# Kernel tuning notes

Measured on AMD Instinct MI355X. Metric: run time of the kernel, lower is better.

Reference implementation:

```python
import jax, jax.numpy as jnp
import numpy as np

B, S, HID = 2, 2048, 1024
NH, DK, DV = 4, 256, 256   # head_k_dim = head_v_dim = 1024 / 4
KSZ = 4                    # conv_size
EPS = 1e-5


def causal_conv1d(x, w):
    # x: [B, S, C] channels-last, w: [C, K] depthwise kernel (torch [C,1,K] squeezed)
    K = w.shape[1]
    Sn = x.shape[1]
    xp = jnp.pad(x, ((0, 0), (K - 1, 0), (0, 0)))
    # cross-correlation with left padding K-1 -> causal: out[t] = sum_j w[:,j] * x[t-(K-1)+j]
    out = xp[:, 0:Sn, :] * w[:, 0]
    for j in range(1, K):
        out = out + xp[:, j:j + Sn, :] * w[:, j]
    return out


def l2norm(x, eps=1e-6):
    return x * jax.lax.rsqrt(jnp.sum(x * x, axis=-1, keepdims=True) + eps)


def rms_norm(x, w, eps=EPS):
    return x * jax.lax.rsqrt(jnp.mean(x * x, axis=-1, keepdims=True) + eps) * w


def delta_rule(q, k, v, beta):
    # q,k: [B,S,H,dk]; v: [B,S,H,dv]; beta: [B,S,H]
    Bn, Sn, Hn, dk = q.shape
    dv = v.shape[-1]
    N = Bn * Hn
    qs = jnp.moveaxis(q, 1, 0).reshape(Sn, N, dk)
    ks = jnp.moveaxis(k, 1, 0).reshape(Sn, N, dk)
    vs = jnp.moveaxis(v, 1, 0).reshape(Sn, N, dv)
    bs = jnp.moveaxis(beta, 1, 0).reshape(Sn, N)

    S0 = jnp.zeros((N, dk, dv), q.dtype)

    def step(St, inp):
        qt, kt, vt, bt = inp
        kS = jnp.einsum('nk,nkv->nv', kt, St)              # k^T S
        St = St + jnp.einsum('nk,nv->nkv', kt, bt[:, None] * (vt - kS))
        ot = jnp.einsum('nk,nkv->nv', qt, St)
        return St, ot

    _, o = jax.lax.scan(step, S0, (qs, ks, vs, bs))        # o: [S, N, dv]
    o = o.reshape(Sn, Bn, Hn, dv)
    return jnp.moveaxis(o, 0, 1)                            # [B,S,H,dv]


def setup_inputs() -> dict:
    key = jax.random.key(0)
    ks = jax.random.split(key, 10)
    w_scale = 2.0 ** (-2.5) * np.sqrt(6.0 / (HID + HID))   # xavier_uniform with gain 2^-2.5
    u = lambda k, shp, s: jax.random.uniform(k, shp, jnp.float32, -s, s)
    return {
        'hidden_states': jax.random.normal(ks[0], (B, S, HID), jnp.float32),
        'Wq': u(ks[1], (HID, NH * DK), w_scale),
        'Wk': u(ks[2], (HID, NH * DK), w_scale),
        'Wv': u(ks[3], (HID, NH * DV), w_scale),
        'Wb': u(ks[4], (HID, NH), w_scale),
        'conv_q': jax.random.normal(ks[5], (NH * DK, KSZ), jnp.float32) * 0.2,
        'conv_k': jax.random.normal(ks[6], (NH * DK, KSZ), jnp.float32) * 0.2,
        'conv_v': jax.random.normal(ks[7], (NH * DV, KSZ), jnp.float32) * 0.2,
        'norm_w': jnp.ones((DV,), jnp.float32),
        'Wo': u(ks[8], (NH * DV, HID), w_scale),
    }


def reference(hidden_states, Wq, Wk, Wv, Wb, conv_q, conv_k, conv_v, norm_w, Wo):
    q = hidden_states @ Wq                                  # [B,S,key_dim]
    k = hidden_states @ Wk
    v = hidden_states @ Wv
    q = causal_conv1d(q, conv_q)
    k = causal_conv1d(k, conv_k)
    v = causal_conv1d(v, conv_v)
    q = jax.nn.silu(q).reshape(B, S, NH, DK)
    k = jax.nn.silu(k).reshape(B, S, NH, DK)
    v = jax.nn.silu(v).reshape(B, S, NH, DV)
    beta = jax.nn.sigmoid(hidden_states @ Wb)               # [B,S,H]
    q = l2norm(q)
    k = l2norm(k)
    o = delta_rule(q, k, v, beta)                           # [B,S,H,dv]
    o = rms_norm(o, norm_w)
    o = o.reshape(B, S, NH * DV) @ Wo                       # [B,S,HID]
    return o
```

## Files before the change

kernel.cpp:

```cpp
#include <hip/hip_runtime.h>
#include <math.h>

#define BB   2
#define SS   2048
#define HIDD 1024
#define ROWS 4096
#define NCH  32
#define CH   64

typedef unsigned short u16t;
typedef unsigned int   u32t;

typedef __attribute__((ext_vector_type(8))) short bf16x8;
typedef __attribute__((ext_vector_type(4))) float f32x4;

__device__ __forceinline__ float bf2f(u16t u) { return __uint_as_float(((u32t)u) << 16); }
__device__ __forceinline__ u16t f2bf(float f) {
    u32t b = __float_as_uint(f);
    return (u16t)((b + 0x7FFFu + ((b >> 16) & 1u)) >> 16);
}
__device__ __forceinline__ float lo_bf(u32t u) { return __uint_as_float(u << 16); }
__device__ __forceinline__ float hi_bf(u32t u) { return __uint_as_float(u & 0xFFFF0000u); }

__device__ __forceinline__ float waveReduceSum(float v) {
#pragma unroll
    for (int m = 1; m < 64; m <<= 1) v += __shfl_xor(v, m, 64);
    return v;
}

__device__ __forceinline__ void gload16(const void* g, void* l) {
    __builtin_amdgcn_global_load_lds(
        (const __attribute__((address_space(1))) unsigned int*)g,
        (__attribute__((address_space(3))) unsigned int*)l, 16, 0, 0);
}

#define MFMA(a, b, c) __builtin_amdgcn_mfma_f32_16x16x32_bf16(a, b, c, 0, 0, 0)

__global__ __launch_bounds__(256) void f2bf_kernel(const float* __restrict__ in,
                                                   u16t* __restrict__ out) {
    const size_t idx = ((size_t)blockIdx.x * 256 + threadIdx.x) * 8;
    float4 a = *(const float4*)&in[idx];
    float4 b = *(const float4*)&in[idx + 4];
    ushort4 o1, o2;
    o1.x = f2bf(a.x); o1.y = f2bf(a.y); o1.z = f2bf(a.z); o1.w = f2bf(a.w);
    o2.x = f2bf(b.x); o2.y = f2bf(b.y); o2.z = f2bf(b.z); o2.w = f2bf(b.w);
    *(ushort4*)&out[idx] = o1;
    *(ushort4*)&out[idx + 4] = o2;
}

__global__ __launch_bounds__(256) void transpose_w4(const float* __restrict__ W0,
                                                    const float* __restrict__ W1,
                                                    const float* __restrict__ W2,
                                                    const float* __restrict__ W3,
                                                    u16t* __restrict__ T0,
                                                    u16t* __restrict__ T1,
                                                    u16t* __restrict__ T2,
                                                    u16t* __restrict__ T3) {
    __shared__ u16t tile[64][65];
    const int z = blockIdx.z;
    const float* W = (z == 0) ? W0 : (z == 1) ? W1 : (z == 2) ? W2 : W3;
    u16t* WT = (z == 0) ? T0 : (z == 1) ? T1 : (z == 2) ? T2 : T3;
    const int t = threadIdx.x;
    const int r0 = blockIdx.y * 64, c0 = blockIdx.x * 64;
    const int lr = t >> 2, lc4 = (t & 3) * 16;
#pragma unroll
    for (int m = 0; m < 4; ++m) {
        float4 v = *(const float4*)&W[(size_t)(r0 + lr) * 1024 + c0 + lc4 + m * 4];
        tile[lr][lc4 + m * 4 + 0] = f2bf(v.x);
        tile[lr][lc4 + m * 4 + 1] = f2bf(v.y);
        tile[lr][lc4 + m * 4 + 2] = f2bf(v.z);
        tile[lr][lc4 + m * 4 + 3] = f2bf(v.w);
    }
    __syncthreads();
#pragma unroll
    for (int m = 0; m < 16; ++m)
        WT[(size_t)(c0 + lr) * 1024 + r0 + lc4 + m] = tile[lc4 + m][lr];
}

__global__ __launch_bounds__(256) void gemm_mfma(const u16t* __restrict__ A,
                                                 const u16t* __restrict__ BT,
                                                 float* __restrict__ Cf,
                                                 u16t* __restrict__ Cb, int obf,
                                                 int M, int N, int K,
                                                 size_t bStrideP, size_t cStrideP) {
    __shared__ u16t As[128 * 64];
    __shared__ u16t Bs[128 * 64];
    const int t = threadIdx.x, l = t & 63, w = t >> 6;
    const int wr = w >> 1, wc = w & 1;
    const int rowBase = blockIdx.y * 128, colBase = blockIdx.x * 128;
    const int l15 = l & 15, g4 = l >> 4;

    const int bplane = colBase >> 10;
    const int bcol = colBase & 1023;

    const int srow = l >> 3;
    const int sj = (l & 7) ^ srow;
    const u16t* aSrc = A + (size_t)(rowBase + srow) * K + sj * 8;
    const u16t* bSrc = BT + (size_t)bplane * bStrideP + (size_t)(bcol + srow) * K + sj * 8;

    f32x4 acc[4][4];
#pragma unroll
    for (int i = 0; i < 4; ++i)
#pragma unroll
        for (int j = 0; j < 4; ++j) acc[i][j] = (f32x4){0.f, 0.f, 0.f, 0.f};

    for (int k0 = 0; k0 < K; k0 += 64) {
#pragma unroll
        for (int i = 0; i < 4; ++i) {
            const int rb = (i * 4 + w) * 8;
            gload16(aSrc + (size_t)rb * K + k0, &As[rb * 64]);
            gload16(bSrc + (size_t)rb * K + k0, &Bs[rb * 64]);
        }
        __syncthreads();
#pragma unroll
        for (int kh = 0; kh < 2; ++kh) {
            bf16x8 aF[4], bF[4];
#pragma unroll
            for (int mi = 0; mi < 4; ++mi) {
                const int row = wr * 64 + mi * 16 + l15;
                const int phys = (kh * 4 + g4) ^ (row & 7);
                aF[mi] = *(const bf16x8*)&As[row * 64 + phys * 8];
            }
#pragma unroll
            for (int ni = 0; ni < 4; ++ni) {
                const int row = wc * 64 + ni * 16 + l15;
                const int phys = (kh * 4 + g4) ^ (row & 7);
                bF[ni] = *(const bf16x8*)&Bs[row * 64 + phys * 8];
            }
#pragma unroll
            for (int mi = 0; mi < 4; ++mi)
#pragma unroll
                for (int ni = 0; ni < 4; ++ni)
                    acc[mi][ni] = MFMA(aF[mi], bF[ni], acc[mi][ni]);
        }
        __syncthreads();
    }
#pragma unroll
    for (int mi = 0; mi < 4; ++mi)
#pragma unroll
        for (int ni = 0; ni < 4; ++ni)
#pragma unroll
            for (int rg = 0; rg < 4; ++rg) {
                const int row = rowBase + wr * 64 + mi * 16 + g4 * 4 + rg;
                const int col = colBase + wc * 64 + ni * 16 + l15;
                const int plane = col >> 10, cc = col & 1023;
                const float v = acc[mi][ni][rg];
                if (obf) Cb[(size_t)plane * cStrideP + (size_t)row * 1024 + cc] = f2bf(v);
                else     Cf[(size_t)plane * cStrideP + (size_t)row * 1024 + cc] = v;
            }
}

__global__ __launch_bounds__(256) void beta_kernel(const float* __restrict__ X,
                                                   const float* __restrict__ Wb,
                                                   float* __restrict__ beta) {
    const int gw   = (blockIdx.x * blockDim.x + threadIdx.x) >> 6;
    const int lane = threadIdx.x & 63;
    if (gw >= ROWS) return;
    const float* x = X + (size_t)gw * HIDD;
    float a0 = 0.f, a1 = 0.f, a2 = 0.f, a3 = 0.f;
#pragma unroll
    for (int i = 0; i < 4; ++i) {
        const int k = lane * 16 + i * 4;
        float4 xv = *(const float4*)&x[k];
        float4 w0 = *(const float4*)&Wb[(size_t)(k + 0) * 4];
        float4 w1 = *(const float4*)&Wb[(size_t)(k + 1) * 4];
        float4 w2 = *(const float4*)&Wb[(size_t)(k + 2) * 4];
        float4 w3 = *(const float4*)&Wb[(size_t)(k + 3) * 4];
        a0 += xv.x * w0.x + xv.y * w1.x + xv.z * w2.x + xv.w * w3.x;
        a1 += xv.x * w0.y + xv.y * w1.y + xv.z * w2.y + xv.w * w3.y;
        a2 += xv.x * w0.z + xv.y * w1.z + xv.z * w2.z + xv.w * w3.z;
        a3 += xv.x * w0.w + xv.y * w1.w + xv.z * w2.w + xv.w * w3.w;
    }
    a0 = waveReduceSum(a0); a1 = waveReduceSum(a1);
    a2 = waveReduceSum(a2); a3 = waveReduceSum(a3);
    if (lane == 0) {
        float4 o = make_float4(1.f / (1.f + expf(-a0)), 1.f / (1.f + expf(-a1)),
                               1.f / (1.f + expf(-a2)), 1.f / (1.f + expf(-a3)));
        *(float4*)&beta[(size_t)gw * 4] = o;
    }
}

__global__ __launch_bounds__(256) void conv_qv(const u16t* __restrict__ inQ,
                                               const float* __restrict__ wQ,
                                               u16t* __restrict__ outQ,
                                               const u16t* __restrict__ inV,
                                               const float* __restrict__ wV,
                                               u16t* __restrict__ outV) {
    const int isQ = (blockIdx.y == 0);
    const u16t* in = isQ ? inQ : inV;
    const float* w = isQ ? wQ : wV;
    u16t* out      = isQ ? outQ : outV;
    const int doL2 = isQ;

    const int gw   = (blockIdx.x * blockDim.x + threadIdx.x) >> 6;
    const int lane = threadIdx.x & 63;
    const int r = gw >> 2;
    const int h = gw & 3;
    const int b = r >> 11;
    const int s = r & 2047;
    const int c4 = h * 256 + lane * 4;

    const float4 wr0 = *(const float4*)&w[(size_t)(c4 + 0) * 4];
    const float4 wr1 = *(const float4*)&w[(size_t)(c4 + 1) * 4];
    const float4 wr2 = *(const float4*)&w[(size_t)(c4 + 2) * 4];
    const float4 wr3 = *(const float4*)&w[(size_t)(c4 + 3) * 4];

    const size_t rowB = (size_t)(b << 11);
    float x0[4] = {0, 0, 0, 0}, x1[4] = {0, 0, 0, 0}, x2[4] = {0, 0, 0, 0}, x3[4];
    ushort4 u;
    if (s >= 3) { u = *(const ushort4*)&in[(rowB + s - 3) * HIDD + c4];
        x0[0] = bf2f(u.x); x0[1] = bf2f(u.y); x0[2] = bf2f(u.z); x0[3] = bf2f(u.w); }
    if (s >= 2) { u = *(const ushort4*)&in[(rowB + s - 2) * HIDD + c4];
        x1[0] = bf2f(u.x); x1[1] = bf2f(u.y); x1[2] = bf2f(u.z); x1[3] = bf2f(u.w); }
    if (s >= 1) { u = *(const ushort4*)&in[(rowB + s - 1) * HIDD + c4];
        x2[0] = bf2f(u.x); x2[1] = bf2f(u.y); x2[2] = bf2f(u.z); x2[3] = bf2f(u.w); }
    u = *(const ushort4*)&in[(rowB + s) * HIDD + c4];
    x3[0] = bf2f(u.x); x3[1] = bf2f(u.y); x3[2] = bf2f(u.z); x3[3] = bf2f(u.w);

    float y0 = wr0.x * x0[0] + wr0.y * x1[0] + wr0.z * x2[0] + wr0.w * x3[0];
    float y1 = wr1.x * x0[1] + wr1.y * x1[1] + wr1.z * x2[1] + wr1.w * x3[1];
    float y2 = wr2.x * x0[2] + wr2.y * x1[2] + wr2.z * x2[2] + wr2.w * x3[2];
    float y3 = wr3.x * x0[3] + wr3.y * x1[3] + wr3.z * x2[3] + wr3.w * x3[3];

    y0 = y0 / (1.f + expf(-y0)); y1 = y1 / (1.f + expf(-y1));
    y2 = y2 / (1.f + expf(-y2)); y3 = y3 / (1.f + expf(-y3));

    if (doL2) {
        float ss = y0 * y0 + y1 * y1 + y2 * y2 + y3 * y3;
        ss = waveReduceSum(ss);
        float sc = rsqrtf(ss + 1e-6f);
        y0 *= sc; y1 *= sc; y2 *= sc; y3 *= sc;
    }
    ushort4 o;
    o.x = f2bf(y0); o.y = f2bf(y1); o.z = f2bf(y2); o.w = f2bf(y3);
    *(ushort4*)&out[(size_t)r * HIDD + c4] = o;
}

__global__ __launch_bounds__(256) void conv_k_chunk(const u16t* __restrict__ pre,
                                                    const float* __restrict__ w,
                                                    u16t* __restrict__ rowout,
                                                    u16t* __restrict__ trout) {
    const int t = threadIdx.x;
    const int bh = blockIdx.x >> 5, c = blockIdx.x & 31;
    const int b = bh >> 2, h = bh & 3;
    const int i = t >> 2, g = t & 3;
    const int s = c * 64 + i;
    const size_t row = (size_t)b * 2048 + s;
    const int ch0 = h * 256 + g * 64;
    const int cloc = g * 64;
    float y[64];
#pragma unroll
    for (int m = 0; m < 8; ++m) {
        const int cm = ch0 + m * 8;
        uint4 x3 = *(const uint4*)&pre[row * 1024 + cm];
        uint4 x2 = (s >= 1) ? *(const uint4*)&pre[(row - 1) * 1024 + cm] : make_uint4(0, 0, 0, 0);
        uint4 x1 = (s >= 2) ? *(const uint4*)&pre[(row - 2) * 1024 + cm] : make_uint4(0, 0, 0, 0);
        uint4 x0 = (s >= 3) ? *(const uint4*)&pre[(row - 3) * 1024 + cm] : make_uint4(0, 0, 0, 0);
        u32t c0[4] = {x0.x, x0.y, x0.z, x0.w};
        u32t c1[4] = {x1.x, x1.y, x1.z, x1.w};
        u32t c2[4] = {x2.x, x2.y, x2.z, x2.w};
        u32t c3[4] = {x3.x, x3.y, x3.z, x3.w};
#pragma unroll
        for (int p = 0; p < 4; ++p) {
            const int ch = m * 8 + p * 2;
            float4 wA = *(const float4*)&w[(size_t)(ch0 + ch) * 4];
            float4 wB = *(const float4*)&w[(size_t)(ch0 + ch + 1) * 4];
            float ya = wA.x * lo_bf(c0[p]) + wA.y * lo_bf(c1[p]) + wA.z * lo_bf(c2[p]) + wA.w * lo_bf(c3[p]);
            float yb = wB.x * hi_bf(c0[p]) + wB.y * hi_bf(c1[p]) + wB.z * hi_bf(c2[p]) + wB.w * hi_bf(c3[p]);
            ya = ya / (1.f + expf(-ya));
            yb = yb / (1.f + expf(-yb));
            y[ch] = ya; y[ch + 1] = yb;
        }
    }
    float ss = 0.f;
#pragma unroll
    for (int e = 0; e < 64; ++e) ss += y[e] * y[e];
    ss += __shfl_xor(ss, 1);
    ss += __shfl_xor(ss, 2);
    const float sc = rsqrtf(ss + 1e-6f);
#pragma unroll
    for (int m = 0; m < 8; ++m) {
        uint4 o;
        u32t* op = (u32t*)&o;
#pragma unroll
        for (int p = 0; p < 4; ++p) {
            u16t a = f2bf(y[m * 8 + p * 2] * sc);
            u16t bb2 = f2bf(y[m * 8 + p * 2 + 1] * sc);
            op[p] = (u32t)a | ((u32t)bb2 << 16);
        }
        *(uint4*)&rowout[row * 1024 + ch0 + m * 8] = o;
    }
#pragma unroll
    for (int e = 0; e < 64; ++e)
        trout[((size_t)bh * 256 + cloc + e) * 2048 + s] = f2bf(y[e] * sc);
}

__global__ __launch_bounds__(256) void prep_kernel(const u16t* __restrict__ qcb,
                                                   const u16t* __restrict__ kcb,
                                                   const float* __restrict__ beta,
                                                   u16t* __restrict__ Tghi,
                                                   u16t* __restrict__ Tglo,
                                                   u16t* __restrict__ Agb) {
    __shared__ float KT[256][68];
    __shared__ float QT[256][68];
    __shared__ float Af[64][68];
    const int t = threadIdx.x;
    const int bhc = blockIdx.x;
    const int bh = bhc >> 5, c = bhc & 31;
    const int b = bh >> 2, h = bh & 3;
    const int tb = b * SS + c * CH;

    {
        const int i = t & 63, rb = t >> 6;
        const u16t* kg = kcb + (size_t)(tb + i) * HIDD + h * 256 + rb * 64;
        const u16t* qg = qcb + (size_t)(tb + i) * HIDD + h * 256 + rb * 64;
#pragma unroll
        for (int m = 0; m < 8; ++m) {
            uint4 kv = ((const uint4*)kg)[m];
            uint4 qv = ((const uint4*)qg)[m];
            u32t kw[4] = {kv.x, kv.y, kv.z, kv.w};
            u32t qw[4] = {qv.x, qv.y, qv.z, qv.w};
#pragma unroll
            for (int n = 0; n < 4; ++n) {
                int rr = rb * 64 + m * 8 + n * 2;
                KT[rr][i]     = lo_bf(kw[n]);
                KT[rr + 1][i] = hi_bf(kw[n]);
                QT[rr][i]     = lo_bf(qw[n]);
                QT[rr + 1][i] = hi_bf(qw[n]);
            }
        }
    }
    __syncthreads();

    const int it = t & 63, jb = t >> 6;
    float kk[16], qk[16];
#pragma unroll
    for (int m = 0; m < 16; ++m) { kk[m] = 0.f; qk[m] = 0.f; }
#pragma unroll 2
    for (int r = 0; r < 256; ++r) {
        float ki = KT[r][it];
        float qi = QT[r][it];
        float4 ka = *(const float4*)&KT[r][jb * 16 + 0];
        float4 kb = *(const float4*)&KT[r][jb * 16 + 4];
        float4 kc = *(const float4*)&KT[r][jb * 16 + 8];
        float4 kd = *(const float4*)&KT[r][jb * 16 + 12];
        float kj[16] = {ka.x, ka.y, ka.z, ka.w, kb.x, kb.y, kb.z, kb.w,
                        kc.x, kc.y, kc.z, kc.w, kd.x, kd.y, kd.z, kd.w};
#pragma unroll
        for (int m = 0; m < 16; ++m) { kk[m] += ki * kj[m]; qk[m] += qi * kj[m]; }
    }

    const float bta = beta[(size_t)(tb + it) * 4 + h];
    u16t* ag = Agb + (size_t)bhc * 4096 + (size_t)it * 64 + jb * 16;
#pragma unroll
    for (int m = 0; m < 16; ++m) {
        int j = jb * 16 + m;
        Af[it][j] = (j < it) ? bta * kk[m] : 0.f;
    }
#pragma unroll
    for (int m4 = 0; m4 < 4; ++m4) {
        ushort4 o;
        o.x = f2bf((jb * 16 + m4 * 4 + 0 <= it) ? qk[m4 * 4 + 0] : 0.f);
        o.y = f2bf((jb * 16 + m4 * 4 + 1 <= it) ? qk[m4 * 4 + 1] : 0.f);
        o.z = f2bf((jb * 16 + m4 * 4 + 2 <= it) ? qk[m4 * 4 + 2] : 0.f);
        o.w = f2bf((jb * 16 + m4 * 4 + 3 <= it) ? qk[m4 * 4 + 3] : 0.f);
        *(ushort4*)&ag[m4 * 4] = o;
    }
    __syncthreads();

    if (t < 64) {
        const int ccol = t;
        float tc[64];
#pragma unroll
        for (int j = 0; j < 64; ++j) tc[j] = (j == ccol) ? 1.f : 0.f;
#pragma unroll
        for (int i = 1; i < 64; ++i) {
            float a = 0.f;
#pragma unroll
            for (int j = 0; j < i; ++j) a += Af[i][j] * tc[j];
            tc[i] -= a;
        }
        u16t* th = Tghi + (size_t)bhc * 4096;
        u16t* tl = Tglo + (size_t)bhc * 4096;
#pragma unroll
        for (int i = 0; i < 64; ++i) {
            u16t hi = f2bf(tc[i]);
            th[i * 64 + ccol] = hi;
            tl[i * 64 + ccol] = f2bf(tc[i] - bf2f(hi));
        }
    }
}

__global__ __launch_bounds__(256, 1) void scan_mfma(const u16t* __restrict__ qcb,
                                                    const u16t* __restrict__ kcb,
                                                    const u16t* __restrict__ ktr,
                                                    const u16t* __restrict__ vcb,
                                                    const float* __restrict__ beta,
                                                    const u16t* __restrict__ TghiG,
                                                    const u16t* __restrict__ TgloG,
                                                    const u16t* __restrict__ AgbG,
                                                    u16t* __restrict__ o_raw) {
    __shared__ u16t Shi[16 * 256];
    __shared__ u16t Slo[16 * 256];
    __shared__ u16t Rhi[16 * 64];
    __shared__ u16t Rlo[16 * 64];
    __shared__ u16t Uhi[16 * 64];
    __shared__ u16t Ulo[16 * 64];

    const int t = threadIdx.x, l = t & 63, w = t >> 6;
    const int bh = blockIdx.x & 7, vt = blockIdx.x >> 3;
    const int b = bh >> 2, h = bh & 3;
    const int vcol0 = vt * 16;
    const int vlow = l & 15, g4 = l >> 4;

    for (int i = t; i < 16 * 256; i += 256) { Shi[i] = 0; Slo[i] = 0; }
    f32x4 sf[4];
#pragma unroll
    for (int q = 0; q < 4; ++q) sf[q] = (f32x4){0.f, 0.f, 0.f, 0.f};

    bf16x8 kf[8], qf[8], tfh[2], tfl[2], af[2], kcf[8];
    u16t vfb[4];
    float bta[4];

    auto loadKQ = [&](int c) {
        const size_t rb = (size_t)(b * 2048 + c * 64 + 16 * w + vlow) * 1024 + h * 256 + g4 * 8;
#pragma unroll
        for (int ks = 0; ks < 8; ++ks) {
            kf[ks] = *(const bf16x8*)(kcb + rb + ks * 32);
            qf[ks] = *(const bf16x8*)(qcb + rb + ks * 32);
        }
    };
    auto loadVB = [&](int c) {
        const int r0 = b * 2048 + c * 64 + 16 * w + 4 * g4;
#pragma unroll
        for (int rg = 0; rg < 4; ++rg) {
            vfb[rg] = vcb[(size_t)(r0 + rg) * 1024 + h * 256 + vcol0 + vlow];
            bta[rg] = beta[(size_t)(r0 + rg) * 4 + h];
        }
    };
    auto loadT = [&](int c) {
        const size_t tb2 = (size_t)(bh * 32 + c) * 4096 + (size_t)(16 * w + vlow) * 64 + g4 * 8;
        tfh[0] = *(const bf16x8*)(TghiG + tb2);
        tfh[1] = *(const bf16x8*)(TghiG + tb2 + 32);
        tfl[0] = *(const bf16x8*)(TgloG + tb2);
        tfl[1] = *(const bf16x8*)(TgloG + tb2 + 32);
    };
    auto loadA = [&](int c) {
        const size_t tb2 = (size_t)(bh * 32 + c) * 4096 + (size_t)(16 * w + vlow) * 64 + g4 * 8;
        af[0] = *(const bf16x8*)(AgbG + tb2);
        af[1] = *(const bf16x8*)(AgbG + tb2 + 32);
    };
    auto loadKC = [&](int c) {
        const size_t cb2 = ((size_t)bh * 256 + 64 * w + vlow) * 2048 + c * 64 + g4 * 8;
#pragma unroll
        for (int q2 = 0; q2 < 4; ++q2) {
            kcf[q2 * 2 + 0] = *(const bf16x8*)(ktr + cb2 + (size_t)(16 * q2) * 2048);
            kcf[q2 * 2 + 1] = *(const bf16x8*)(ktr + cb2 + (size_t)(16 * q2) * 2048 + 32);
        }
    };

    loadKQ(0); loadVB(0); loadT(0); loadA(0); loadKC(0);
    __syncthreads();

    for (int c = 0; c < NCH; ++c) {
        const int cn = (c + 1 < NCH) ? c + 1 : c;
        const int trow0 = b * 2048 + c * 64;

        f32x4 Wacc = (f32x4){0.f, 0.f, 0.f, 0.f};
        f32x4 O1   = (f32x4){0.f, 0.f, 0.f, 0.f};
#pragma unroll
        for (int ks = 0; ks < 8; ++ks) {
            const int pb = (((ks * 4 + g4) ^ (vlow & 7)) << 3);
            bf16x8 bH = *(const bf16x8*)&Shi[vlow * 256 + pb];
            bf16x8 bL = *(const bf16x8*)&Slo[vlow * 256 + pb];
            Wacc = MFMA(kf[ks], bH, Wacc); Wacc = MFMA(kf[ks], bL, Wacc);
            O1   = MFMA(qf[ks], bH, O1);   O1   = MFMA(qf[ks], bL, O1);
        }
        {
            const int tslot = 2 * w + (g4 >> 1);
            const int base = vlow * 64 + ((tslot ^ (vlow & 7)) << 3) + ((g4 & 1) << 2);
            u16t rh[4], rl[4];
#pragma unroll
            for (int rg = 0; rg < 4; ++rg) {
                float rv = bta[rg] * (bf2f(vfb[rg]) - Wacc[rg]);
                rh[rg] = f2bf(rv);
                rl[rg] = f2bf(rv - bf2f(rh[rg]));
            }
            uint2 ph, pl;
            ph.x = (u32t)rh[0] | ((u32t)rh[1] << 16); ph.y = (u32t)rh[2] | ((u32t)rh[3] << 16);
            pl.x = (u32t)rl[0] | ((u32t)rl[1] << 16); pl.y = (u32t)rl[2] | ((u32t)rl[3] << 16);
            *(uint2*)&Rhi[base] = ph;
            *(uint2*)&Rlo[base] = pl;
        }
        loadKQ(cn);
        loadVB(cn);
        __syncthreads();

        f32x4 Uacc = (f32x4){0.f, 0.f, 0.f, 0.f};
#pragma unroll
        for (int ks = 0; ks < 2; ++ks) {
            const int pb = (((ks * 4 + g4) ^ (vlow & 7)) << 3);
            bf16x8 bH = *(const bf16x8*)&Rhi[vlow * 64 + pb];
            bf16x8 bL = *(const bf16x8*)&Rlo[vlow * 64 + pb];
            Uacc = MFMA(tfh[ks], bH, Uacc);
            Uacc = MFMA(tfh[ks], bL, Uacc);
            Uacc = MFMA(tfl[ks], bH, Uacc);
        }
        {
            const int tslot = 2 * w + (g4 >> 1);
            const int base = vlow * 64 + ((tslot ^ (vlow & 7)) << 3) + ((g4 & 1) << 2);
            u16t uh[4], ul[4];
#pragma unroll
            for (int rg = 0; rg < 4; ++rg) {
                uh[rg] = f2bf(Uacc[rg]);
                ul[rg] = f2bf(Uacc[rg] - bf2f(uh[rg]));
            }
            uint2 ph, pl;
            ph.x = (u32t)uh[0] | ((u32t)uh[1] << 16); ph.y = (u32t)uh[2] | ((u32t)uh[3] << 16);
            pl.x = (u32t)ul[0] | ((u32t)ul[1] << 16); pl.y = (u32t)ul[2] | ((u32t)ul[3] << 16);
            *(uint2*)&Uhi[base] = ph;
            *(uint2*)&Ulo[base] = pl;
        }
        loadT(cn);
        __syncthreads();

        bf16x8 uhf[2], ulf[2];
#pragma unroll
        for (int ks = 0; ks < 2; ++ks) {
            const int pb = (((ks * 4 + g4) ^ (vlow & 7)) << 3);
            uhf[ks] = *(const bf16x8*)&Uhi[vlow * 64 + pb];
            ulf[ks] = *(const bf16x8*)&Ulo[vlow * 64 + pb];
        }
        f32x4 Oacc = O1;
#pragma unroll
        for (int ks = 0; ks < 2; ++ks) {
            Oacc = MFMA(af[ks], uhf[ks], Oacc);
            Oacc = MFMA(af[ks], ulf[ks], Oacc);
        }
#pragma unroll
        for (int rg = 0; rg < 4; ++rg)
            o_raw[(size_t)(trow0 + 16 * w + 4 * g4 + rg) * 1024 + h * 256 + vcol0 + vlow] = f2bf(Oacc[rg]);
        loadA(cn);

#pragma unroll
        for (int q = 0; q < 4; ++q) {
#pragma unroll
            for (int ks = 0; ks < 2; ++ks) {
                sf[q] = MFMA(kcf[q * 2 + ks], uhf[ks], sf[q]);
                sf[q] = MFMA(kcf[q * 2 + ks], ulf[ks], sf[q]);
            }
        }
        loadKC(cn);

#pragma unroll
        for (int q = 0; q < 4; ++q) {
            u16t sh[4], sl[4];
#pragma unroll
            for (int rg = 0; rg < 4; ++rg) {
                u16t hi = f2bf(sf[q][rg]);
                sh[rg] = hi;
                sl[rg] = f2bf(sf[q][rg] - bf2f(hi));
            }
            const int rslot = 8 * w + 2 * q + (g4 >> 1);
            const int base = vlow * 256 + ((rslot ^ (vlow & 7)) << 3) + ((g4 & 1) << 2);
            uint2 ph, pl;
            ph.x = (u32t)sh[0] | ((u32t)sh[1] << 16); ph.y = (u32t)sh[2] | ((u32t)sh[3] << 16);
            pl.x = (u32t)sl[0] | ((u32t)sl[1] << 16); pl.y = (u32t)sl[2] | ((u32t)sl[3] << 16);
            *(uint2*)&Shi[base] = ph;
            *(uint2*)&Slo[base] = pl;
        }
        __syncthreads();
    }
}

__global__ __launch_bounds__(256) void rms_kernel(const u16t* __restrict__ in,
                                                  const float* __restrict__ w,
                                                  u16t* __restrict__ out) {
    const int gw   = (blockIdx.x * blockDim.x + threadIdx.x) >> 6;
    const int lane = threadIdx.x & 63;
    const int r = gw >> 2;
    const int h = gw & 3;
    const size_t base = (size_t)r * HIDD + h * 256 + lane * 4;
    ushort4 xv = *(const ushort4*)&in[base];
    float x0 = bf2f(xv.x), x1 = bf2f(xv.y), x2 = bf2f(xv.z), x3 = bf2f(xv.w);
    float ss = x0 * x0 + x1 * x1 + x2 * x2 + x3 * x3;
    ss = waveReduceSum(ss);
    const float sc = rsqrtf(ss * (1.0f / 256.0f) + 1e-5f);
    float4 wv = *(const float4*)&w[lane * 4];
    ushort4 o;
    o.x = f2bf(x0 * sc * wv.x); o.y = f2bf(x1 * sc * wv.y);
    o.z = f2bf(x2 * sc * wv.z); o.w = f2bf(x3 * sc * wv.w);
    *(ushort4*)&out[base] = o;
}

extern "C" void kernel_launch(void* const* d_in, const int* in_sizes, int n_in,
                              void* d_out, int out_size, void* d_ws, size_t ws_size,
                              hipStream_t stream) {
    const float* X      = (const float*)d_in[0];
    const float* Wq     = (const float*)d_in[1];
    const float* Wk     = (const float*)d_in[2];
    const float* Wv     = (const float*)d_in[3];
    const float* Wb     = (const float*)d_in[4];
    const float* conv_q = (const float*)d_in[5];
    const float* conv_k = (const float*)d_in[6];
    const float* conv_v = (const float*)d_in[7];
    const float* norm_w = (const float*)d_in[8];
    const float* Wo     = (const float*)d_in[9];
    float* out = (float*)d_out;

    char* W8 = (char*)d_ws;
    const size_t MB = 1u << 20;
    u16t* Xbf   = (u16t*)(W8 + 0 * MB);
    u16t* o_raw = Xbf;
    u16t* qpre  = (u16t*)(W8 + 8 * MB);
    u16t* o_nrm = qpre;
    u16t* kpre  = (u16t*)(W8 + 16 * MB);
    u16t* Tghi  = (u16t*)(W8 + 16 * MB);
    u16t* Tglo  = (u16t*)(W8 + 18 * MB);
    u16t* Agb   = (u16t*)(W8 + 20 * MB);
    u16t* vpre  = (u16t*)(W8 + 24 * MB);
    u16t* ktr   = (u16t*)(W8 + 24 * MB);
    u16t* WqT   = (u16t*)(W8 + 32 * MB);
    u16t* qcb   = (u16t*)(W8 + 32 * MB);
    u16t* WkT   = (u16t*)(W8 + 40 * MB);
    u16t* kcb   = (u16t*)(W8 + 40 * MB);
    u16t* WvT   = (u16t*)(W8 + 48 * MB);
    u16t* vcb   = (u16t*)(W8 + 48 * MB);
    u16t* WoT   = (u16t*)(W8 + 56 * MB);
    float* betab = (float*)(W8 + 58 * MB);

    const size_t PL = 4194304;

    f2bf_kernel<<<2048, 256, 0, stream>>>(X, Xbf);
    transpose_w4<<<dim3(16, 16, 4), 256, 0, stream>>>(Wq, Wk, Wv, Wo, WqT, WkT, WvT, WoT);

    gemm_mfma<<<dim3(24, 32), 256, 0, stream>>>(Xbf, WqT, nullptr, qpre, 1,
                                                ROWS, 3072, HIDD, PL, PL);
    beta_kernel<<<ROWS / 4, 256, 0, stream>>>(X, Wb, betab);

    conv_qv<<<dim3(ROWS, 2), 256, 0, stream>>>(qpre, conv_q, qcb, vpre, conv_v, vcb);
    conv_k_chunk<<<256, 256, 0, stream>>>(kpre, conv_k, kcb, ktr);

    prep_kernel<<<256, 256, 0, stream>>>(qcb, kcb, betab, Tghi, Tglo, Agb);
    scan_mfma<<<128, 256, 0, stream>>>(qcb, kcb, ktr, vcb, betab, Tghi, Tglo, Agb, o_raw);

    rms_kernel<<<ROWS, 256, 0, stream>>>(o_raw, norm_w, o_nrm);
    gemm_mfma<<<dim3(8, 32), 256, 0, stream>>>(o_nrm, WoT, out, nullptr, 0,
                                               ROWS, HIDD, HIDD, 0, 0);
}
```

Measured before the change: 286.7 us.

## Pack four value-tile groups into one 1024-thread scan block

The chunked delta-rule scan now launches 32 blocks of 1024 threads instead of 128 blocks of 256. Each block holds four independent 4-wave groups, one per 16-column value tile, each with its own slice of shared state. Groups with the same (b,h) share the same K/Q/T/A chunk data, so cache reuse may improve. The cost is that __syncthreads now makes all 16 waves wait on each other even though the groups are independent, and only 32 CUs are occupied.

```diff
diff --git a/kernel.cpp b/kernel.cpp
--- a/kernel.cpp
+++ b/kernel.cpp
@@ -391,29 +391,38 @@
     }
 }
 
-__global__ __launch_bounds__(256, 1) void scan_mfma(const u16t* __restrict__ qcb,
-                                                    const u16t* __restrict__ kcb,
-                                                    const u16t* __restrict__ ktr,
-                                                    const u16t* __restrict__ vcb,
-                                                    const float* __restrict__ beta,
-                                                    const u16t* __restrict__ TghiG,
-                                                    const u16t* __restrict__ TgloG,
-                                                    const u16t* __restrict__ AgbG,
-                                                    u16t* __restrict__ o_raw) {
-    __shared__ u16t Shi[16 * 256];
-    __shared__ u16t Slo[16 * 256];
-    __shared__ u16t Rhi[16 * 64];
-    __shared__ u16t Rlo[16 * 64];
-    __shared__ u16t Uhi[16 * 64];
-    __shared__ u16t Ulo[16 * 64];
+__global__ __launch_bounds__(1024, 1) void scan_mfma(const u16t* __restrict__ qcb,
+                                                     const u16t* __restrict__ kcb,
+                                                     const u16t* __restrict__ ktr,
+                                                     const u16t* __restrict__ vcb,
+                                                     const float* __restrict__ beta,
+                                                     const u16t* __restrict__ TghiG,
+                                                     const u16t* __restrict__ TgloG,
+                                                     const u16t* __restrict__ AgbG,
+                                                     u16t* __restrict__ o_raw) {
+    __shared__ u16t Shi[4 * 16 * 256];
+    __shared__ u16t Slo[4 * 16 * 256];
+    __shared__ u16t Rhi[4 * 16 * 64];
+    __shared__ u16t Rlo[4 * 16 * 64];
+    __shared__ u16t Uhi[4 * 16 * 64];
+    __shared__ u16t Ulo[4 * 16 * 64];
 
     const int t = threadIdx.x, l = t & 63, w = t >> 6;
-    const int bh = blockIdx.x & 7, vt = blockIdx.x >> 3;
+    const int grp = w >> 2, wv = w & 3;
+    const int bh = blockIdx.x & 7;
+    const int vt = (blockIdx.x >> 3) * 4 + grp;
     const int b = bh >> 2, h = bh & 3;
     const int vcol0 = vt * 16;
     const int vlow = l & 15, g4 = l >> 4;
 
-    for (int i = t; i < 16 * 256; i += 256) { Shi[i] = 0; Slo[i] = 0; }
+    u16t* gShi = Shi + grp * (16 * 256);
+    u16t* gSlo = Slo + grp * (16 * 256);
+    u16t* gRhi = Rhi + grp * (16 * 64);
+    u16t* gRlo = Rlo + grp * (16 * 64);
+    u16t* gUhi = Uhi + grp * (16 * 64);
+    u16t* gUlo = Ulo + grp * (16 * 64);
+
+    for (int i = t; i < 4 * 16 * 256; i += 1024) { Shi[i] = 0; Slo[i] = 0; }
     f32x4 sf[4];
 #pragma unroll
     for (int q = 0; q < 4; ++q) sf[q] = (f32x4){0.f, 0.f, 0.f, 0.f};
@@ -423,7 +432,7 @@
     float bta[4];
 
     auto loadKQ = [&](int c) {
-        const size_t rb = (size_t)(b * 2048 + c * 64 + 16 * w + vlow) * 1024 + h * 256 + g4 * 8;
+        const size_t rb = (size_t)(b * 2048 + c * 64 + 16 * wv + vlow) * 1024 + h * 256 + g4 * 8;
 #pragma unroll
         for (int ks = 0; ks < 8; ++ks) {
             kf[ks] = *(const bf16x8*)(kcb + rb + ks * 32);
@@ -431,7 +440,7 @@
         }
     };
     auto loadVB = [&](int c) {
-        const int r0 = b * 2048 + c * 64 + 16 * w + 4 * g4;
+        const int r0 = b * 2048 + c * 64 + 16 * wv + 4 * g4;
 #pragma unroll
         for (int rg = 0; rg < 4; ++rg) {
             vfb[rg] = vcb[(size_t)(r0 + rg) * 1024 + h * 256 + vcol0 + vlow];
@@ -439,19 +448,19 @@
         }
     };
     auto loadT = [&](int c) {
-        const size_t tb2 = (size_t)(bh * 32 + c) * 4096 + (size_t)(16 * w + vlow) * 64 + g4 * 8;
+        const size_t tb2 = (size_t)(bh * 32 + c) * 4096 + (size_t)(16 * wv + vlow) * 64 + g4 * 8;
         tfh[0] = *(const bf16x8*)(TghiG + tb2);
         tfh[1] = *(const bf16x8*)(TghiG + tb2 + 32);
         tfl[0] = *(const bf16x8*)(TgloG + tb2);
         tfl[1] = *(const bf16x8*)(TgloG + tb2 + 32);
     };
     auto loadA = [&](int c) {
-        const size_t tb2 = (size_t)(bh * 32 + c) * 4096 + (size_t)(16 * w + vlow) * 64 + g4 * 8;
+        const size_t tb2 = (size_t)(bh * 32 + c) * 4096 + (size_t)(16 * wv + vlow) * 64 + g4 * 8;
         af[0] = *(const bf16x8*)(AgbG + tb2);
         af[1] = *(const bf16x8*)(AgbG + tb2 + 32);
     };
     auto loadKC = [&](int c) {
-        const size_t cb2 = ((size_t)bh * 256 + 64 * w + vlow) * 2048 + c * 64 + g4 * 8;
+        const size_t cb2 = ((size_t)bh * 256 + 64 * wv + vlow) * 2048 + c * 64 + g4 * 8;
 #pragma unroll
         for (int q2 = 0; q2 < 4; ++q2) {
             kcf[q2 * 2 + 0] = *(const bf16x8*)(ktr + cb2 + (size_t)(16 * q2) * 2048);
@@ -471,13 +480,13 @@
 #pragma unroll
         for (int ks = 0; ks < 8; ++ks) {
             const int pb = (((ks * 4 + g4) ^ (vlow & 7)) << 3);
-            bf16x8 bH = *(const bf16x8*)&Shi[vlow * 256 + pb];
-            bf16x8 bL = *(const bf16x8*)&Slo[vlow * 256 + pb];
+            bf16x8 bH = *(const bf16x8*)&gShi[vlow * 256 + pb];
+            bf16x8 bL = *(const bf16x8*)&gSlo[vlow * 256 + pb];
             Wacc = MFMA(kf[ks], bH, Wacc); Wacc = MFMA(kf[ks], bL, Wacc);
             O1   = MFMA(qf[ks], bH, O1);   O1   = MFMA(qf[ks], bL, O1);
         }
         {
-            const int tslot = 2 * w + (g4 >> 1);
+            const int tslot = 2 * wv + (g4 >> 1);
             const int base = vlow * 64 + ((tslot ^ (vlow & 7)) << 3) + ((g4 & 1) << 2);
             u16t rh[4], rl[4];
 #pragma unroll
@@ -489,8 +498,8 @@
             uint2 ph, pl;
             ph.x = (u32t)rh[0] | ((u32t)rh[1] << 16); ph.y = (u32t)rh[2] | ((u32t)rh[3] << 16);
             pl.x = (u32t)rl[0] | ((u32t)rl[1] << 16); pl.y = (u32t)rl[2] | ((u32t)rl[3] << 16);
-            *(uint2*)&Rhi[base] = ph;
-            *(uint2*)&Rlo[base] = pl;
+            *(uint2*)&gRhi[base] = ph;
+            *(uint2*)&gRlo[base] = pl;
         }
         loadKQ(cn);
         loadVB(cn);
@@ -500,14 +509,14 @@
 #pragma unroll
         for (int ks = 0; ks < 2; ++ks) {
             const int pb = (((ks * 4 + g4) ^ (vlow & 7)) << 3);
-            bf16x8 bH = *(const bf16x8*)&Rhi[vlow * 64 + pb];
-            bf16x8 bL = *(const bf16x8*)&Rlo[vlow * 64 + pb];
+            bf16x8 bH = *(const bf16x8*)&gRhi[vlow * 64 + pb];
+            bf16x8 bL = *(const bf16x8*)&gRlo[vlow * 64 + pb];
             Uacc = MFMA(tfh[ks], bH, Uacc);
             Uacc = MFMA(tfh[ks], bL, Uacc);
             Uacc = MFMA(tfl[ks], bH, Uacc);
         }
         {
-            const int tslot = 2 * w + (g4 >> 1);
+            const int tslot = 2 * wv + (g4 >> 1);
             const int base = vlow * 64 + ((tslot ^ (vlow & 7)) << 3) + ((g4 & 1) << 2);
             u16t uh[4], ul[4];
 #pragma unroll
@@ -518,8 +527,8 @@
             uint2 ph, pl;
             ph.x = (u32t)uh[0] | ((u32t)uh[1] << 16); ph.y = (u32t)uh[2] | ((u32t)uh[3] << 16);
             pl.x = (u32t)ul[0] | ((u32t)ul[1] << 16); pl.y = (u32t)ul[2] | ((u32t)ul[3] << 16);
-            *(uint2*)&Uhi[base] = ph;
-            *(uint2*)&Ulo[base] = pl;
+            *(uint2*)&gUhi[base] = ph;
+            *(uint2*)&gUlo[base] = pl;
         }
         loadT(cn);
         __syncthreads();
@@ -528,8 +537,8 @@
 #pragma unroll
         for (int ks = 0; ks < 2; ++ks) {
             const int pb = (((ks * 4 + g4) ^ (vlow & 7)) << 3);
-            uhf[ks] = *(const bf16x8*)&Uhi[vlow * 64 + pb];
-            ulf[ks] = *(const bf16x8*)&Ulo[vlow * 64 + pb];
+            uhf[ks] = *(const bf16x8*)&gUhi[vlow * 64 + pb];
+            ulf[ks] = *(const bf16x8*)&gUlo[vlow * 64 + pb];
         }
         f32x4 Oacc = O1;
 #pragma unroll
@@ -539,7 +548,7 @@
         }
 #pragma unroll
         for (int rg = 0; rg < 4; ++rg)
-            o_raw[(size_t)(trow0 + 16 * w + 4 * g4 + rg) * 1024 + h * 256 + vcol0 + vlow] = f2bf(Oacc[rg]);
+            o_raw[(size_t)(trow0 + 16 * wv + 4 * g4 + rg) * 1024 + h * 256 + vcol0 + vlow] = f2bf(Oacc[rg]);
         loadA(cn);
 
 #pragma unroll
@@ -561,13 +570,13 @@
                 sh[rg] = hi;
                 sl[rg] = f2bf(sf[q][rg] - bf2f(hi));
             }
-            const int rslot = 8 * w + 2 * q + (g4 >> 1);
+            const int rslot = 8 * wv + 2 * q + (g4 >> 1);
             const int base = vlow * 256 + ((rslot ^ (vlow & 7)) << 3) + ((g4 & 1) << 2);
             uint2 ph, pl;
             ph.x = (u32t)sh[0] | ((u32t)sh[1] << 16); ph.y = (u32t)sh[2] | ((u32t)sh[3] << 16);
             pl.x = (u32t)sl[0] | ((u32t)sl[1] << 16); pl.y = (u32t)sl[2] | ((u32t)sl[3] << 16);
-            *(uint2*)&Shi[base] = ph;
-            *(uint2*)&Slo[base] = pl;
+            *(uint2*)&gShi[base] = ph;
+            *(uint2*)&gSlo[base] = pl;
         }
         __syncthreads();
     }
@@ -642,7 +651,7 @@
     conv_k_chunk<<<256, 256, 0, stream>>>(kpre, conv_k, kcb, ktr);
 
     prep_kernel<<<256, 256, 0, stream>>>(qcb, kcb, betab, Tghi, Tglo, Agb);
-    scan_mfma<<<128, 256, 0, stream>>>(qcb, kcb, ktr, vcb, betab, Tghi, Tglo, Agb, o_raw);
+    scan_mfma<<<32, 1024, 0, stream>>>(qcb, kcb, ktr, vcb, betab, Tghi, Tglo, Agb, o_raw);
 
     rms_kernel<<<ROWS, 256, 0, stream>>>(o_raw, norm_w, o_nrm);
     gemm_mfma<<<dim3(8, 32), 256, 0, stream>>>(o_nrm, WoT, out, nullptr, 0,
```

Result: slower. 975.6 us (+240.3%).
